# Optimization experiments

Measured on AMD Instinct MI355X. Metric: run time of the kernel, lower is better.

## Reference

```python
import jax, jax.numpy as jnp
import numpy as np

B, T, I, H, D1, D2 = 16384, 512, 3, 15, 64, 64


def setup_inputs() -> dict:
    key = jax.random.key(0)
    ks = jax.random.split(key, 9)
    s = 1.0 / np.sqrt(H)  # torch default uniform bound for LSTM/Linear(15,...)
    u = lambda k, shape, bound: jax.random.uniform(k, shape, jnp.float32, -bound, bound)
    return {
        "x": jax.random.normal(ks[0], (B, T, I), jnp.float32),
        "W_ih": u(ks[1], (4 * H, I), s),
        "W_hh": u(ks[2], (4 * H, H), s),
        "b_ih": u(ks[3], (4 * H,), s),
        "b_hh": u(ks[4], (4 * H,), s),
        "W1": u(ks[5], (D1, H), s),
        "b1": u(ks[6], (D1,), s),
        "W2": u(ks[7], (D2, D1), 1.0 / np.sqrt(D1)),
        "b2": u(ks[8], (D2,), 1.0 / np.sqrt(D1)),
    }


def reference(x, W_ih, W_hh, b_ih, b_hh, W1, b1, W2, b2):
    # Single-layer LSTM (torch gate order: i, f, g, o), keep only last h.
    b = b_ih + b_hh  # [4H]
    batch = x.shape[0]

    def step(carry, xt):
        h, c = carry  # [B,H] each
        gates = xt @ W_ih.T + h @ W_hh.T + b  # [B,4H]
        i, f, g, o = jnp.split(gates, 4, axis=-1)
        c = jax.nn.sigmoid(f) * c + jax.nn.sigmoid(i) * jnp.tanh(g)
        h = jax.nn.sigmoid(o) * jnp.tanh(c)
        return (h, c), None

    h0 = jnp.zeros((batch, H), x.dtype)
    c0 = jnp.zeros((batch, H), x.dtype)
    (h_last, _), _ = jax.lax.scan(step, (h0, c0), jnp.swapaxes(x, 0, 1))  # scan over T

    # Head: Linear(15,64) -> ReLU -> Linear(64,64) (no ReLU after last layer)
    y = jax.nn.relu(h_last @ W1.T + b1)
    return y @ W2.T + b2  # [B, 64]
```

## Files before the change

kernel.cpp:

```cpp
#include <hip/hip_runtime.h>
#include <hip/hip_bf16.h>

#define B_TOT 16384
#define T_LEN 512

typedef float f32x4 __attribute__((ext_vector_type(4)));
typedef short bf16x8 __attribute__((ext_vector_type(8)));
typedef unsigned int u32;
typedef u32 u32x4 __attribute__((ext_vector_type(4)));

#define LOG2E 1.4426950408889634f

__device__ __forceinline__ float fast_rcp(float x) { return __builtin_amdgcn_rcpf(x); }
__device__ __forceinline__ float exp2_hw(float x) {
  float r;
  asm("v_exp_f32 %0, %1" : "=v"(r) : "v"(x));
  return r;
}

__device__ __forceinline__ unsigned short f32_to_bf16_rne(float f) {
  u32 u = __float_as_uint(f);
  u = u + 0x7fffu + ((u >> 16) & 1u);
  return (unsigned short)(u >> 16);
}
__device__ __forceinline__ float bf16u_to_f32(unsigned short s) {
  return __uint_as_float(((u32)s) << 16);
}
__device__ __forceinline__ u32 cvt_pk_bf16(float a, float b) {
  u32 r;
  asm("v_cvt_pk_bf16_f32 %0, %1, %2" : "=v"(r) : "v"(a), "v"(b));
  return r;
}

__global__ __launch_bounds__(256, 1) void lstm_scan_mfma(
    const float* __restrict__ x, const float* __restrict__ W_ih,
    const float* __restrict__ W_hh, const float* __restrict__ b_ih,
    const float* __restrict__ b_hh, float* __restrict__ h_out) {
  const int tid = threadIdx.x;
  const int lane = tid & 63;
  const int wave = tid >> 6;
  const int hi = lane >> 4;
  const int cs = lane & 15;
  const int seq = blockIdx.x * 64 + wave * 16 + cs;
  const int u = cs;

  bf16x8 A1[4], A2[4];
  f32x4 cbias[4];
#pragma unroll
  for (int g = 0; g < 4; ++g) {
    const float gs = (g == 2) ? (2.0f * LOG2E) : (-LOG2E);
#pragma unroll
    for (int e = 0; e < 8; ++e) {
      const int k = 8 * hi + e;
      const int kk = k & 15;
      float w1 = (u < 15 && kk < 15) ? gs * W_hh[(g * 15 + u) * 15 + kk] : 0.0f;
      A1[g][e] = (short)f32_to_bf16_rne(w1);
      float v = 0.0f;
      if (u < 15) {
        if (k < 15) {
          float w = gs * W_hh[(g * 15 + u) * 15 + k];
          v = w - bf16u_to_f32(f32_to_bf16_rne(w));
        } else if (k >= 16 && k <= 18) {
          v = gs * W_ih[(g * 15 + u) * 3 + (k - 16)];
        } else if (k >= 19 && k <= 21) {
          v = gs * W_ih[(g * 15 + u) * 3 + (k - 19)];
        } else if (k >= 22 && k <= 24) {
          float w = gs * W_ih[(g * 15 + u) * 3 + (k - 22)];
          v = w - bf16u_to_f32(f32_to_bf16_rne(w));
        }
      }
      A2[g][e] = (short)f32_to_bf16_rne(v);
    }
#pragma unroll
    for (int r = 0; r < 4; ++r) {
      const int uu = 4 * hi + r;
      cbias[g][r] = (uu < 15) ? gs * (b_ih[g * 15 + uu] + b_hh[g * 15 + uu]) : 0.0f;
    }
  }

  float carr[4] = {0.0f, 0.0f, 0.0f, 0.0f};
  float harr[4] = {0.0f, 0.0f, 0.0f, 0.0f};
  u32 w0 = 0u, w1 = 0u, w2 = 0u, w3 = 0u;

  const float* xb = x + (size_t)seq * (T_LEN * 3);
  float nx0 = xb[0], nx1 = xb[1], nx2 = xb[2];

  const bool lo_half = (hi < 2);
  const bool is2 = (hi == 2);

  for (int t = 0; t < T_LEN; ++t) {
    const float xc0 = nx0, xc1 = nx1, xc2 = nx2;
    {
      const int tn = (t + 1 < T_LEN) ? (t + 1) : t;
      nx0 = xb[tn * 3 + 0];
      nx1 = xb[tn * 3 + 1];
      nx2 = xb[tn * 3 + 2];
    }

    const u32 xr0 = cvt_pk_bf16(xc0, xc1);
    const float xh0 = __uint_as_float(xr0 << 16);
    const float xh1 = __uint_as_float(xr0 & 0xffff0000u);
    const float xl0 = xc0 - xh0;
    const float xl1 = xc1 - xh1;
    const u32 xr1 = cvt_pk_bf16(xc2, xl0);
    const float xh2 = __uint_as_float(xr1 << 16);
    const float xl2 = xc2 - xh2;
    const u32 xr2 = cvt_pk_bf16(xl1, xl2);
    const u32 xt0 = xr1 & 0x0000ffffu;

    const u32 q0 = lo_half ? w0 : (is2 ? xr0 : xt0);
    const u32 q1 = lo_half ? w1 : (is2 ? xr1 : 0u);
    const u32 q2 = lo_half ? w2 : (is2 ? xr2 : 0u);
    const u32 q3 = lo_half ? w3 : (is2 ? xr0 : 0u);
    const bf16x8 Bf1 = __builtin_bit_cast(bf16x8, (u32x4){w0, w1, w2, w3});
    const bf16x8 Bf2 = __builtin_bit_cast(bf16x8, (u32x4){q0, q1, q2, q3});

    f32x4 acc0 = __builtin_amdgcn_mfma_f32_16x16x32_bf16(A1[0], Bf1, cbias[0], 0, 0, 0);
    f32x4 acc1 = __builtin_amdgcn_mfma_f32_16x16x32_bf16(A1[1], Bf1, cbias[1], 0, 0, 0);
    f32x4 acc2 = __builtin_amdgcn_mfma_f32_16x16x32_bf16(A1[2], Bf1, cbias[2], 0, 0, 0);
    f32x4 acc3 = __builtin_amdgcn_mfma_f32_16x16x32_bf16(A1[3], Bf1, cbias[3], 0, 0, 0);
    acc0 = __builtin_amdgcn_mfma_f32_16x16x32_bf16(A2[0], Bf2, acc0, 0, 0, 0);
    acc1 = __builtin_amdgcn_mfma_f32_16x16x32_bf16(A2[1], Bf2, acc1, 0, 0, 0);
    acc2 = __builtin_amdgcn_mfma_f32_16x16x32_bf16(A2[2], Bf2, acc2, 0, 0, 0);
    acc3 = __builtin_amdgcn_mfma_f32_16x16x32_bf16(A2[3], Bf2, acc3, 0, 0, 0);

#pragma unroll
    for (int r = 0; r < 4; ++r) {
      const float Di = 1.0f + exp2_hw(acc0[r]);
      const float Df = 1.0f + exp2_hw(acc1[r]);
      const float Dg = 1.0f + exp2_hw(acc2[r]);
      const float Do = 1.0f + exp2_hw(acc3[r]);
      const float r1 = fast_rcp(Di * Df);
      const float ig = r1 * Df;
      const float fg = r1 * Di;
      const float r2 = fast_rcp(Dg * Do);
      const float tg = fmaf(-2.0f, r2 * Do, 1.0f);
      const float og = r2 * Dg;
      carr[r] = fmaf(fg, carr[r], ig * tg);
      const float cs2 = carr[r] * (2.0f * LOG2E);
      const float tc = fmaf(-2.0f, fast_rcp(1.0f + exp2_hw(cs2)), 1.0f);
      harr[r] = og * tc;
    }

    u32 ph0 = cvt_pk_bf16(harr[0], harr[1]);
    u32 ph1 = cvt_pk_bf16(harr[2], harr[3]);
    const float e0 = harr[0] - __uint_as_float(ph0 << 16);
    const float e1 = harr[1] - __uint_as_float(ph0 & 0xffff0000u);
    const float e2 = harr[2] - __uint_as_float(ph1 << 16);
    const float e3 = harr[3] - __uint_as_float(ph1 & 0xffff0000u);
    u32 pl0 = cvt_pk_bf16(e0, e1);
    u32 pl1 = cvt_pk_bf16(e2, e3);

    asm volatile(
        "s_nop 1\n\t"
        "v_permlane32_swap_b32 %0, %2\n\t"
        "v_permlane32_swap_b32 %1, %3\n\t"
        "s_nop 0\n\t"
        "v_permlane16_swap_b32 %0, %2\n\t"
        "v_permlane16_swap_b32 %1, %3"
        : "+v"(ph0), "+v"(ph1), "+v"(pl0), "+v"(pl1));
    w0 = ph0;
    w1 = ph1;
    w2 = pl0;
    w3 = pl1;
  }

  float4 outv = make_float4(harr[0], harr[1], harr[2], harr[3]);
  *reinterpret_cast<float4*>(h_out + (size_t)seq * 16 + 4 * hi) = outv;
}

__global__ __launch_bounds__(256) void head_mlp_kernel(
    const float* __restrict__ h_ws, const float* __restrict__ W1,
    const float* __restrict__ b1, const float* __restrict__ W2,
    const float* __restrict__ b2, float* __restrict__ out) {
  __shared__ float sW1[64][17];
  __shared__ float sW2[64][65];
  __shared__ float sh[64][17];
  __shared__ float sy[64][65];
  __shared__ float sb1[64];
  __shared__ float sb2[64];

  const int tid = threadIdx.x;
  for (int i = tid; i < 64 * 16; i += 256) {
    const int u = i >> 4, k = i & 15;
    sW1[u][k] = (k < 15) ? W1[u * 15 + k] : 0.0f;
  }
  if (tid < 64) {
    sb1[tid] = b1[tid];
    sb2[tid] = b2[tid];
  }
  for (int i = tid; i < 64 * 64; i += 256) sW2[i >> 6][i & 63] = W2[i];
  for (int i = tid; i < 64 * 16; i += 256) sh[i >> 4][i & 15] = h_ws[(size_t)blockIdx.x * 1024 + i];
  __syncthreads();

  const int r = tid >> 2;
  const int q = tid & 3;

  float y1v[16];
#pragma unroll
  for (int j = 0; j < 16; ++j) {
    const int u = q * 16 + j;
    float a = sb1[u];
#pragma unroll
    for (int k = 0; k < 15; ++k) a = fmaf(sW1[u][k], sh[r][k], a);
    y1v[j] = fmaxf(a, 0.0f);
  }
#pragma unroll
  for (int j = 0; j < 16; ++j) sy[r][q * 16 + j] = y1v[j];
  __syncthreads();

  float yv[64];
#pragma unroll
  for (int k = 0; k < 64; ++k) yv[k] = sy[r][k];
  float o[16];
#pragma unroll
  for (int j = 0; j < 16; ++j) {
    const int u = q * 16 + j;
    float a = sb2[u];
#pragma unroll
    for (int k = 0; k < 64; ++k) a = fmaf(sW2[u][k], yv[k], a);
    o[j] = a;
  }

  float* op = out + ((size_t)(blockIdx.x * 64 + r)) * 64 + q * 16;
#pragma unroll
  for (int j = 0; j < 16; ++j) op[j] = o[j];
}

extern "C" void kernel_launch(void* const* d_in, const int* in_sizes, int n_in,
                              void* d_out, int out_size, void* d_ws, size_t ws_size,
                              hipStream_t stream) {
  (void)in_sizes;
  (void)n_in;
  (void)out_size;
  (void)ws_size;
  const float* x = (const float*)d_in[0];
  const float* W_ih = (const float*)d_in[1];
  const float* W_hh = (const float*)d_in[2];
  const float* b_ih = (const float*)d_in[3];
  const float* b_hh = (const float*)d_in[4];
  const float* W1 = (const float*)d_in[5];
  const float* b1 = (const float*)d_in[6];
  const float* W2 = (const float*)d_in[7];
  const float* b2 = (const float*)d_in[8];
  float* out = (float*)d_out;
  float* h_ws = (float*)d_ws;

  lstm_scan_mfma<<<B_TOT / 64, 256, 0, stream>>>(x, W_ih, W_hh, b_ih, b_hh, h_ws);
  head_mlp_kernel<<<B_TOT / 64, 256, 0, stream>>>(h_ws, W1, b1, W2, b2, out);
}
```

Baseline: 237.2 us.

## Precompute input projection one step ahead and shorten recurrent MFMA chain

Moves the x·W_ih plus bias contribution into a separate MFMA issued one timestep ahead, so it sits off the recurrent dependency chain. Each step now needs only one dependent MFMA per gate on h. The B operand now carries h as bf16 duplicated across both k halves, with W_hh split into high and low bf16 parts, replacing the old W_hh-high plus residual layout. The low-order bf16 residual of h is no longer fed to the matmul, so the recurrent state is effectively bf16, which risks accuracy drift over 512 steps. The time loop is unrolled by two to ping-pong the precomputed projection buffers.

```diff
diff --git a/kernel.cpp b/kernel.cpp
--- a/kernel.cpp
+++ b/kernel.cpp
@@ -17,7 +17,6 @@
   asm("v_exp_f32 %0, %1" : "=v"(r) : "v"(x));
   return r;
 }
-
 __device__ __forceinline__ unsigned short f32_to_bf16_rne(float f) {
   u32 u = __float_as_uint(f);
   u = u + 0x7fffu + ((u >> 16) & 1u);
@@ -44,7 +43,7 @@
   const int seq = blockIdx.x * 64 + wave * 16 + cs;
   const int u = cs;
 
-  bf16x8 A1[4], A2[4];
+  bf16x8 Ah[4], Ax[4];
   f32x4 cbias[4];
 #pragma unroll
   for (int g = 0; g < 4; ++g) {
@@ -52,24 +51,28 @@
 #pragma unroll
     for (int e = 0; e < 8; ++e) {
       const int k = 8 * hi + e;
-      const int kk = k & 15;
-      float w1 = (u < 15 && kk < 15) ? gs * W_hh[(g * 15 + u) * 15 + kk] : 0.0f;
-      A1[g][e] = (short)f32_to_bf16_rne(w1);
-      float v = 0.0f;
+      float vh = 0.0f, vx = 0.0f;
       if (u < 15) {
-        if (k < 15) {
-          float w = gs * W_hh[(g * 15 + u) * 15 + k];
-          v = w - bf16u_to_f32(f32_to_bf16_rne(w));
-        } else if (k >= 16 && k <= 18) {
-          v = gs * W_ih[(g * 15 + u) * 3 + (k - 16)];
-        } else if (k >= 19 && k <= 21) {
-          v = gs * W_ih[(g * 15 + u) * 3 + (k - 19)];
-        } else if (k >= 22 && k <= 24) {
-          float w = gs * W_ih[(g * 15 + u) * 3 + (k - 22)];
-          v = w - bf16u_to_f32(f32_to_bf16_rne(w));
+        if (k < 16) {
+          if (k < 15) vh = bf16u_to_f32(f32_to_bf16_rne(gs * W_hh[(g * 15 + u) * 15 + k]));
+        } else {
+          const int kk = k - 16;
+          if (kk < 15) {
+            const float w = gs * W_hh[(g * 15 + u) * 15 + kk];
+            vh = w - bf16u_to_f32(f32_to_bf16_rne(w));
+          }
+        }
+        if (k < 3) {
+          vx = gs * W_ih[(g * 15 + u) * 3 + k];
+        } else if (k < 6) {
+          vx = gs * W_ih[(g * 15 + u) * 3 + (k - 3)];
+        } else if (k < 9) {
+          const float w = gs * W_ih[(g * 15 + u) * 3 + (k - 6)];
+          vx = w - bf16u_to_f32(f32_to_bf16_rne(w));
         }
       }
-      A2[g][e] = (short)f32_to_bf16_rne(v);
+      Ah[g][e] = (short)f32_to_bf16_rne(vh);
+      Ax[g][e] = (short)f32_to_bf16_rne(vx);
     }
 #pragma unroll
     for (int r = 0; r < 4; ++r) {
@@ -83,20 +86,9 @@
   u32 w0 = 0u, w1 = 0u, w2 = 0u, w3 = 0u;
 
   const float* xb = x + (size_t)seq * (T_LEN * 3);
-  float nx0 = xb[0], nx1 = xb[1], nx2 = xb[2];
-
-  const bool lo_half = (hi < 2);
-  const bool is2 = (hi == 2);
-
-  for (int t = 0; t < T_LEN; ++t) {
-    const float xc0 = nx0, xc1 = nx1, xc2 = nx2;
-    {
-      const int tn = (t + 1 < T_LEN) ? (t + 1) : t;
-      nx0 = xb[tn * 3 + 0];
-      nx1 = xb[tn * 3 + 1];
-      nx2 = xb[tn * 3 + 2];
-    }
-
+
+  auto make_bx = [&](float xc0, float xc1, float xc2, u32& b0, u32& b1, u32& b2,
+                     u32& b3) __attribute__((always_inline)) {
     const u32 xr0 = cvt_pk_bf16(xc0, xc1);
     const float xh0 = __uint_as_float(xr0 << 16);
     const float xh1 = __uint_as_float(xr0 & 0xffff0000u);
@@ -107,22 +99,48 @@
     const float xl2 = xc2 - xh2;
     const u32 xr2 = cvt_pk_bf16(xl1, xl2);
     const u32 xt0 = xr1 & 0x0000ffffu;
-
-    const u32 q0 = lo_half ? w0 : (is2 ? xr0 : xt0);
-    const u32 q1 = lo_half ? w1 : (is2 ? xr1 : 0u);
-    const u32 q2 = lo_half ? w2 : (is2 ? xr2 : 0u);
-    const u32 q3 = lo_half ? w3 : (is2 ? xr0 : 0u);
-    const bf16x8 Bf1 = __builtin_bit_cast(bf16x8, (u32x4){w0, w1, w2, w3});
-    const bf16x8 Bf2 = __builtin_bit_cast(bf16x8, (u32x4){q0, q1, q2, q3});
-
-    f32x4 acc0 = __builtin_amdgcn_mfma_f32_16x16x32_bf16(A1[0], Bf1, cbias[0], 0, 0, 0);
-    f32x4 acc1 = __builtin_amdgcn_mfma_f32_16x16x32_bf16(A1[1], Bf1, cbias[1], 0, 0, 0);
-    f32x4 acc2 = __builtin_amdgcn_mfma_f32_16x16x32_bf16(A1[2], Bf1, cbias[2], 0, 0, 0);
-    f32x4 acc3 = __builtin_amdgcn_mfma_f32_16x16x32_bf16(A1[3], Bf1, cbias[3], 0, 0, 0);
-    acc0 = __builtin_amdgcn_mfma_f32_16x16x32_bf16(A2[0], Bf2, acc0, 0, 0, 0);
-    acc1 = __builtin_amdgcn_mfma_f32_16x16x32_bf16(A2[1], Bf2, acc1, 0, 0, 0);
-    acc2 = __builtin_amdgcn_mfma_f32_16x16x32_bf16(A2[2], Bf2, acc2, 0, 0, 0);
-    acc3 = __builtin_amdgcn_mfma_f32_16x16x32_bf16(A2[3], Bf2, acc3, 0, 0, 0);
+    b0 = (hi == 0) ? xr0 : ((hi == 1) ? xt0 : 0u);
+    b1 = (hi == 0) ? xr1 : 0u;
+    b2 = (hi == 0) ? xr2 : 0u;
+    b3 = (hi == 0) ? xr0 : 0u;
+  };
+
+  f32x4 pxA[4], pxB[4];
+  {
+    const float x00 = xb[0], x01 = xb[1], x02 = xb[2];
+    u32 b0, b1, b2, b3;
+    make_bx(x00, x01, x02, b0, b1, b2, b3);
+    const bf16x8 Bx = __builtin_bit_cast(bf16x8, (u32x4){b0, b1, b2, b3});
+    pxA[0] = __builtin_amdgcn_mfma_f32_16x16x32_bf16(Ax[0], Bx, cbias[0], 0, 0, 0);
+    pxA[1] = __builtin_amdgcn_mfma_f32_16x16x32_bf16(Ax[1], Bx, cbias[1], 0, 0, 0);
+    pxA[2] = __builtin_amdgcn_mfma_f32_16x16x32_bf16(Ax[2], Bx, cbias[2], 0, 0, 0);
+    pxA[3] = __builtin_amdgcn_mfma_f32_16x16x32_bf16(Ax[3], Bx, cbias[3], 0, 0, 0);
+  }
+  float nx0 = xb[3], nx1 = xb[4], nx2 = xb[5];
+
+  auto step = [&](f32x4(&PX)[4], f32x4(&PXN)[4],
+                  int tcur) __attribute__((always_inline)) {
+    const bf16x8 Bh = __builtin_bit_cast(bf16x8, (u32x4){w0, w1, w2, w3});
+    f32x4 acc0 = __builtin_amdgcn_mfma_f32_16x16x32_bf16(Ah[0], Bh, PX[0], 0, 0, 0);
+    f32x4 acc1 = __builtin_amdgcn_mfma_f32_16x16x32_bf16(Ah[1], Bh, PX[1], 0, 0, 0);
+    f32x4 acc2 = __builtin_amdgcn_mfma_f32_16x16x32_bf16(Ah[2], Bh, PX[2], 0, 0, 0);
+    f32x4 acc3 = __builtin_amdgcn_mfma_f32_16x16x32_bf16(Ah[3], Bh, PX[3], 0, 0, 0);
+
+    {
+      u32 b0, b1, b2, b3;
+      make_bx(nx0, nx1, nx2, b0, b1, b2, b3);
+      const bf16x8 Bx = __builtin_bit_cast(bf16x8, (u32x4){b0, b1, b2, b3});
+      PXN[0] = __builtin_amdgcn_mfma_f32_16x16x32_bf16(Ax[0], Bx, cbias[0], 0, 0, 0);
+      PXN[1] = __builtin_amdgcn_mfma_f32_16x16x32_bf16(Ax[1], Bx, cbias[1], 0, 0, 0);
+      PXN[2] = __builtin_amdgcn_mfma_f32_16x16x32_bf16(Ax[2], Bx, cbias[2], 0, 0, 0);
+      PXN[3] = __builtin_amdgcn_mfma_f32_16x16x32_bf16(Ax[3], Bx, cbias[3], 0, 0, 0);
+    }
+    {
+      const int tn = (tcur + 2 < T_LEN) ? (tcur + 2) : (T_LEN - 1);
+      nx0 = xb[tn * 3 + 0];
+      nx1 = xb[tn * 3 + 1];
+      nx2 = xb[tn * 3 + 2];
+    }
 
 #pragma unroll
     for (int r = 0; r < 4; ++r) {
@@ -144,25 +162,26 @@
 
     u32 ph0 = cvt_pk_bf16(harr[0], harr[1]);
     u32 ph1 = cvt_pk_bf16(harr[2], harr[3]);
-    const float e0 = harr[0] - __uint_as_float(ph0 << 16);
-    const float e1 = harr[1] - __uint_as_float(ph0 & 0xffff0000u);
-    const float e2 = harr[2] - __uint_as_float(ph1 << 16);
-    const float e3 = harr[3] - __uint_as_float(ph1 & 0xffff0000u);
-    u32 pl0 = cvt_pk_bf16(e0, e1);
-    u32 pl1 = cvt_pk_bf16(e2, e3);
-
+    u32 c0, c1;
     asm volatile(
+        "v_mov_b32 %2, %0\n\t"
+        "v_mov_b32 %3, %1\n\t"
         "s_nop 1\n\t"
         "v_permlane32_swap_b32 %0, %2\n\t"
         "v_permlane32_swap_b32 %1, %3\n\t"
         "s_nop 0\n\t"
         "v_permlane16_swap_b32 %0, %2\n\t"
         "v_permlane16_swap_b32 %1, %3"
-        : "+v"(ph0), "+v"(ph1), "+v"(pl0), "+v"(pl1));
+        : "+v"(ph0), "+v"(ph1), "=&v"(c0), "=&v"(c1));
     w0 = ph0;
     w1 = ph1;
-    w2 = pl0;
-    w3 = pl1;
+    w2 = c0;
+    w3 = c1;
+  };
+
+  for (int t = 0; t < T_LEN; t += 2) {
+    step(pxA, pxB, t);
+    step(pxB, pxA, t + 1);
   }
 
   float4 outv = make_float4(harr[0], harr[1], harr[2], harr[3]);
```

New measurement: 226.1 us. 1.05x faster.
